# Optimization experiments

Measured on AMD Instinct MI355X. Metric: run time of the kernel, lower is better.

## Reference

```python
import jax, jax.numpy as jnp
import numpy as np

TEMPERATURE = 0.5

def setup_inputs() -> dict:
    key = jax.random.key(0)
    k1, k2 = jax.random.split(key)
    emb_i = jax.random.normal(k1, (4096, 128), dtype=jnp.float32)
    emb_j = jax.random.normal(k2, (4096, 128), dtype=jnp.float32)
    return {"emb_i": emb_i, "emb_j": emb_j}

def reference(emb_i, emb_j):
    B = emb_i.shape[0]
    eps = 1e-12
    z_i = emb_i / jnp.maximum(jnp.linalg.norm(emb_i, axis=1, keepdims=True), eps)
    z_j = emb_j / jnp.maximum(jnp.linalg.norm(emb_j, axis=1, keepdims=True), eps)
    z = jnp.concatenate([z_i, z_j], axis=0)  # [2B, D]
    # cosine similarity of normalized vectors == dot product (GEMM instead of O(N^2 D) broadcast)
    sim = z @ z.T  # [2B, 2B]
    sim_ij = jnp.einsum('bd,bd->b', z_i, z_j)  # diag(sim, +B)
    positives = jnp.concatenate([sim_ij, sim_ij], axis=0)  # diag(sim,-B) == diag(sim,+B)
    neg_mask = 1.0 - jnp.eye(2 * B, dtype=sim.dtype)
    denom = jnp.sum(neg_mask * jnp.exp(sim / TEMPERATURE), axis=1)  # [2B]
    loss_partial = -(positives / TEMPERATURE - jnp.log(denom))
    return jnp.sum(loss_partial) / (2 * B)
```

## Files before the change

### kernel.cpp

```cpp
#include <hip/hip_runtime.h>
#include <hip/hip_bf16.h>
#include <math.h>

#define BB       4096
#define N2       8192
#define DIMS     128
#define NT       64
#define NJOBS    (NT * (NT + 1) / 2)
#define TILE     128
#define LDS_PAD  8
#define LDS_ROWW (DIMS + LDS_PAD)

#define ZSCALE   1.6986436f
#define DIAG_E2  7.38905609893065f

typedef __attribute__((ext_vector_type(8))) short short8;
typedef __attribute__((ext_vector_type(4))) float float4v;

__global__ __launch_bounds__(256) void norm_kernel(
    const float* __restrict__ emb_i, const float* __restrict__ emb_j,
    __hip_bfloat16* __restrict__ z, float* __restrict__ pos,
    float* __restrict__ denom) {
  if (blockIdx.x < N2 / 256) denom[blockIdx.x * 256 + threadIdx.x] = 0.0f;

  int gw   = (blockIdx.x * blockDim.x + threadIdx.x) >> 6;
  int lane = threadIdx.x & 63;
  if (gw >= BB) return;

  const float2* ei = (const float2*)(emb_i + (size_t)gw * DIMS);
  const float2* ej = (const float2*)(emb_j + (size_t)gw * DIMS);
  float2 a = ei[lane];
  float2 b = ej[lane];

  float sa = a.x * a.x + a.y * a.y;
  float sb = b.x * b.x + b.y * b.y;
  #pragma unroll
  for (int m = 32; m; m >>= 1) {
    sa += __shfl_xor(sa, m, 64);
    sb += __shfl_xor(sb, m, 64);
  }
  float inva = 1.0f / fmaxf(sqrtf(sa), 1e-12f);
  float invb = 1.0f / fmaxf(sqrtf(sb), 1e-12f);

  float zi0 = a.x * inva, zi1 = a.y * inva;
  float zj0 = b.x * invb, zj1 = b.y * invb;

  float p = zi0 * zj0 + zi1 * zj1;
  #pragma unroll
  for (int m = 32; m; m >>= 1) p += __shfl_xor(p, m, 64);
  if (lane == 0) pos[gw] = p;

  __hip_bfloat162* zr_i = (__hip_bfloat162*)(z + (size_t)gw * DIMS);
  __hip_bfloat162* zr_j = (__hip_bfloat162*)(z + (size_t)(gw + BB) * DIMS);
  __hip_bfloat162 vi, vj;
  vi.x = __float2bfloat16(zi0 * ZSCALE); vi.y = __float2bfloat16(zi1 * ZSCALE);
  vj.x = __float2bfloat16(zj0 * ZSCALE); vj.y = __float2bfloat16(zj1 * ZSCALE);
  zr_i[lane] = vi;
  zr_j[lane] = vj;
}

__global__ __launch_bounds__(256, 4) void simloss_sym(
    const __hip_bfloat16* __restrict__ z, float* __restrict__ denom) {
  __shared__ short lds[TILE * LDS_ROWW];
  __shared__ float csum_lds[4][TILE];

  const int tid  = threadIdx.x;
  const int wave = tid >> 6;
  const int lane = tid & 63;
  const int lr   = lane & 15;
  const int quad = lane >> 4;

  const int j = blockIdx.x;
  int I = (int)((129.0f - sqrtf(16641.0f - 8.0f * (float)j)) * 0.5f);
  I = I < 0 ? 0 : (I > NT - 1 ? NT - 1 : I);
  while (I < NT - 1 && (I + 1) * (2 * NT - I) / 2 <= j) ++I;
  while (I > 0 && I * (2 * NT - I + 1) / 2 > j) --I;
  const int J = I + (j - I * (2 * NT - I + 1) / 2);
  const bool diag = (I == J);
  const int R0 = I * TILE;
  const int C0 = J * TILE;

  const ushort* zp = (const ushort*)z;

  short8 afrag[2][4];
  #pragma unroll
  for (int rt = 0; rt < 2; rt++) {
    const int arow = R0 + wave * 32 + rt * 16 + lr;
    const short8* ap = (const short8*)(zp + (size_t)arow * DIMS + quad * 8);
    afrag[rt][0] = ap[0];
    afrag[rt][1] = ap[4];
    afrag[rt][2] = ap[8];
    afrag[rt][3] = ap[12];
  }

  {
    const short8* src = (const short8*)(zp + (size_t)C0 * DIMS);
    #pragma unroll
    for (int i = 0; i < 8; i++) {
      int idx  = tid + 256 * i;
      int row  = idx >> 4;
      int col8 = idx & 15;
      *(short8*)&lds[row * LDS_ROWW + col8 * 8] = src[idx];
    }
  }
  __syncthreads();

  float rowsum[2][4];
  #pragma unroll
  for (int rt = 0; rt < 2; rt++)
    #pragma unroll
    for (int r = 0; r < 4; r++) rowsum[rt][r] = 0.0f;

  #pragma unroll 2
  for (int t = 0; t < 8; t++) {
    const short8* bp = (const short8*)&lds[(t * 16 + lr) * LDS_ROWW + quad * 8];
    short8 b0 = bp[0];
    short8 b1 = bp[4];
    short8 b2 = bp[8];
    short8 b3 = bp[12];
    float ctile = 0.0f;
    #pragma unroll
    for (int rt = 0; rt < 2; rt++) {
      float4v acc = {0.0f, 0.0f, 0.0f, 0.0f};
      acc = __builtin_amdgcn_mfma_f32_16x16x32_bf16(afrag[rt][0], b0, acc, 0, 0, 0);
      acc = __builtin_amdgcn_mfma_f32_16x16x32_bf16(afrag[rt][1], b1, acc, 0, 0, 0);
      acc = __builtin_amdgcn_mfma_f32_16x16x32_bf16(afrag[rt][2], b2, acc, 0, 0, 0);
      acc = __builtin_amdgcn_mfma_f32_16x16x32_bf16(afrag[rt][3], b3, acc, 0, 0, 0);
      #pragma unroll
      for (int r = 0; r < 4; r++) {
        float e = __builtin_amdgcn_exp2f(acc[r]);
        rowsum[rt][r] += e;
        ctile += e;
      }
    }
    if (!diag) {
      ctile += __shfl_xor(ctile, 16, 64);
      ctile += __shfl_xor(ctile, 32, 64);
      if (quad == 0) csum_lds[wave][t * 16 + lr] = ctile;
    }
  }

  #pragma unroll
  for (int m = 1; m < 16; m <<= 1)
    #pragma unroll
    for (int rt = 0; rt < 2; rt++)
      #pragma unroll
      for (int r = 0; r < 4; r++)
        rowsum[rt][r] += __shfl_xor(rowsum[rt][r], m, 64);
  if (lr == 0) {
    #pragma unroll
    for (int rt = 0; rt < 2; rt++)
      #pragma unroll
      for (int r = 0; r < 4; r++)
        atomicAdd(&denom[R0 + wave * 32 + rt * 16 + quad * 4 + r], rowsum[rt][r]);
  }

  if (!diag) {
    __syncthreads();
    if (tid < TILE) {
      float s = csum_lds[0][tid] + csum_lds[1][tid] +
                csum_lds[2][tid] + csum_lds[3][tid];
      atomicAdd(&denom[C0 + tid], s);
    }
  }
}

__global__ __launch_bounds__(256) void finalize(
    const float* __restrict__ denom, const float* __restrict__ pos,
    float* __restrict__ out) {
  __shared__ double sred[256];
  int tid = threadIdx.x;
  double acc = 0.0;
  for (int r = tid; r < N2; r += 256) {
    acc += (double)(logf(denom[r] - DIAG_E2) - 2.0f * pos[r & (BB - 1)]);
  }
  sred[tid] = acc;
  __syncthreads();
  for (int s = 128; s; s >>= 1) {
    if (tid < s) sred[tid] += sred[tid + s];
    __syncthreads();
  }
  if (tid == 0) out[0] = (float)(sred[0] / (double)N2);
}

extern "C" void kernel_launch(void* const* d_in, const int* in_sizes, int n_in,
                              void* d_out, int out_size, void* d_ws, size_t ws_size,
                              hipStream_t stream) {
  const float* emb_i = (const float*)d_in[0];
  const float* emb_j = (const float*)d_in[1];

  __hip_bfloat16* z = (__hip_bfloat16*)d_ws;
  float* pos   = (float*)((char*)d_ws + (size_t)N2 * DIMS * 2);
  float* denom = pos + BB;

  norm_kernel<<<BB / 4, 256, 0, stream>>>(emb_i, emb_j, z, pos, denom);
  simloss_sym<<<NJOBS, 256, 0, stream>>>(z, denom);
  finalize<<<1, 256, 0, stream>>>(denom, pos, (float*)d_out);
}
```

Baseline: 92.31 us.

## Replace denominator atomics with per-tile partial buffer and parallel row reduction

Each tile job now writes its row and column exp-sums into a dedicated slot of a partial-sum buffer instead of issuing float atomicAdds into a shared denominator array. A new multi-block kernel sums the 64 partials per row, applies the log, and writes block partials that a tiny final kernel adds up. The buffer no longer needs zeroing in the norm kernel. This removes atomic contention and the single-block finalize, at the cost of an extra launch and about 2 MB of partial-sum traffic.

```diff
diff --git a/kernel.cpp b/kernel.cpp
--- a/kernel.cpp
+++ b/kernel.cpp
@@ -19,10 +19,7 @@
 
 __global__ __launch_bounds__(256) void norm_kernel(
     const float* __restrict__ emb_i, const float* __restrict__ emb_j,
-    __hip_bfloat16* __restrict__ z, float* __restrict__ pos,
-    float* __restrict__ denom) {
-  if (blockIdx.x < N2 / 256) denom[blockIdx.x * 256 + threadIdx.x] = 0.0f;
-
+    __hip_bfloat16* __restrict__ z, float* __restrict__ pos) {
   int gw   = (blockIdx.x * blockDim.x + threadIdx.x) >> 6;
   int lane = threadIdx.x & 63;
   if (gw >= BB) return;
@@ -60,7 +57,7 @@
 }
 
 __global__ __launch_bounds__(256, 4) void simloss_sym(
-    const __hip_bfloat16* __restrict__ z, float* __restrict__ denom) {
+    const __hip_bfloat16* __restrict__ z, float* __restrict__ P) {
   __shared__ short lds[TILE * LDS_ROWW];
   __shared__ float csum_lds[4][TILE];
 
@@ -148,11 +145,12 @@
       for (int r = 0; r < 4; r++)
         rowsum[rt][r] += __shfl_xor(rowsum[rt][r], m, 64);
   if (lr == 0) {
-    #pragma unroll
-    for (int rt = 0; rt < 2; rt++)
-      #pragma unroll
-      for (int r = 0; r < 4; r++)
-        atomicAdd(&denom[R0 + wave * 32 + rt * 16 + quad * 4 + r], rowsum[rt][r]);
+    float* Prow = P + ((size_t)I * NT + J) * TILE + wave * 32;
+    #pragma unroll
+    for (int rt = 0; rt < 2; rt++) {
+      float4v v = {rowsum[rt][0], rowsum[rt][1], rowsum[rt][2], rowsum[rt][3]};
+      *(float4v*)&Prow[rt * 16 + quad * 4] = v;
+    }
   }
 
   if (!diag) {
@@ -160,27 +158,42 @@
     if (tid < TILE) {
       float s = csum_lds[0][tid] + csum_lds[1][tid] +
                 csum_lds[2][tid] + csum_lds[3][tid];
-      atomicAdd(&denom[C0 + tid], s);
-    }
-  }
-}
-
-__global__ __launch_bounds__(256) void finalize(
-    const float* __restrict__ denom, const float* __restrict__ pos,
-    float* __restrict__ out) {
+      P[((size_t)J * NT + I) * TILE + tid] = s;
+    }
+  }
+}
+
+__global__ __launch_bounds__(256) void reduce_rows(
+    const float* __restrict__ P, const float* __restrict__ pos,
+    double* __restrict__ bpart) {
   __shared__ double sred[256];
-  int tid = threadIdx.x;
-  double acc = 0.0;
-  for (int r = tid; r < N2; r += 256) {
-    acc += (double)(logf(denom[r] - DIAG_E2) - 2.0f * pos[r & (BB - 1)]);
-  }
-  sred[tid] = acc;
+  const int tid = threadIdx.x;
+  const int r   = blockIdx.x * 256 + tid;
+  const int I   = r >> 7;
+  const int rr  = r & (TILE - 1);
+
+  const float* p = P + (size_t)I * NT * TILE + rr;
+  float acc = 0.0f;
+  #pragma unroll 8
+  for (int J = 0; J < NT; J++) acc += p[(size_t)J * TILE];
+
+  double term = (double)(logf(acc - DIAG_E2) - 2.0f * pos[r & (BB - 1)]);
+  sred[tid] = term;
   __syncthreads();
   for (int s = 128; s; s >>= 1) {
     if (tid < s) sred[tid] += sred[tid + s];
     __syncthreads();
   }
-  if (tid == 0) out[0] = (float)(sred[0] / (double)N2);
+  if (tid == 0) bpart[blockIdx.x] = sred[0];
+}
+
+__global__ __launch_bounds__(64) void final_sum(
+    const double* __restrict__ bpart, float* __restrict__ out) {
+  int tid = threadIdx.x;
+  double v = (tid < 32) ? bpart[tid] : 0.0;
+  #pragma unroll
+  for (int m = 32; m; m >>= 1) v += __shfl_xor(v, m, 64);
+  if (tid == 0) out[0] = (float)(v / (double)N2);
 }
 
 extern "C" void kernel_launch(void* const* d_in, const int* in_sizes, int n_in,
@@ -191,9 +204,11 @@
 
   __hip_bfloat16* z = (__hip_bfloat16*)d_ws;
   float* pos   = (float*)((char*)d_ws + (size_t)N2 * DIMS * 2);
-  float* denom = pos + BB;
-
-  norm_kernel<<<BB / 4, 256, 0, stream>>>(emb_i, emb_j, z, pos, denom);
-  simloss_sym<<<NJOBS, 256, 0, stream>>>(z, denom);
-  finalize<<<1, 256, 0, stream>>>(denom, pos, (float*)d_out);
-}
+  float* P     = pos + BB;
+  double* bpart = (double*)(P + (size_t)NT * NT * TILE);
+
+  norm_kernel<<<BB / 4, 256, 0, stream>>>(emb_i, emb_j, z, pos);
+  simloss_sym<<<NJOBS, 256, 0, stream>>>(z, P);
+  reduce_rows<<<N2 / 256, 256, 0, stream>>>(P, pos, bpart);
+  final_sum<<<1, 64, 0, stream>>>(bpart, (float*)d_out);
+}
```

After: 83.81 us. 1.1x faster.
